# Kernel tuning notes

Hardware: AMD Instinct MI355X
Metric: run time of the kernel (lower is better)

Reference implementation:

```python
import jax, jax.numpy as jnp
import numpy as np
from jax import lax

B, C, H, W = 32, 128, 56, 56
O, KS, K = 128, 3, 2
HIDDEN = 32  # int(in_planes * ratio)
TEMPERATURE = 31.0
STRIDE, PAD = 1, 1


def setup_inputs() -> dict:
    key = jax.random.key(0)
    ks = jax.random.split(key, 6)
    return {
        "x": jax.random.normal(ks[0], (B, C, H, W), jnp.float32),
        "common_weight": jax.random.normal(ks[1], (1, O, C, KS, KS), jnp.float32) * 0.05,
        "common_bias": jax.random.normal(ks[2], (1, O), jnp.float32) * 0.05,
        "dyn_weight": jax.random.normal(ks[3], (1, O, C, KS, KS), jnp.float32) * 0.05,
        "dyn_bias": jnp.zeros((1, O), jnp.float32),
        "fc1_w": jax.random.normal(ks[4], (HIDDEN, C), jnp.float32) * 0.1,
        "fc2_w": jax.random.normal(ks[5], (K, HIDDEN), jnp.float32) * 0.1,
    }


def reference(x, common_weight, common_bias, dyn_weight, dyn_bias, fc1_w, fc2_w):
    b, c, h, w = x.shape
    # attention2d: global avg pool -> 1x1 conv -> relu -> 1x1 conv -> softmax(./T)
    pooled = jnp.mean(x, axis=(2, 3))                       # [B, C]
    hid = jax.nn.relu(pooled @ fc1_w.T)                     # [B, hidden]
    logits = hid @ fc2_w.T                                  # [B, K]
    attn = jax.nn.softmax(logits / TEMPERATURE, axis=1)     # [B, K]

    # aggregate per-sample weights/biases from the K-bank
    weight_all = jnp.concatenate([common_weight, dyn_weight], axis=0)  # [K,O,C,k,k]
    agg_w = jnp.einsum('bk,kocij->bocij', attn, weight_all)            # [B,O,C,k,k]
    bias_all = jnp.concatenate([common_bias, dyn_bias], axis=0)       # [K,O]
    agg_b = attn @ bias_all                                            # [B,O]

    # per-sample conv via grouped conv with feature_group_count = batch
    x1 = x.reshape(1, b * c, h, w)
    w1 = agg_w.reshape(b * O, c, KS, KS)
    out = lax.conv_general_dilated(
        x1, w1,
        window_strides=(STRIDE, STRIDE),
        padding=((PAD, PAD), (PAD, PAD)),
        dimension_numbers=('NCHW', 'OIHW', 'NCHW'),
        feature_group_count=b,
    )  # [1, B*O, H', W']
    out = out.reshape(b, O, out.shape[-2], out.shape[-1])
    return out + agg_b[:, :, None, None]
```

## Files before the change

### kernel.cpp

```cpp
#include <hip/hip_runtime.h>


#define B_ 32
#define C_ 128
#define O_ 128
#define SP_ 3136

typedef __bf16  bf16x8 __attribute__((ext_vector_type(8)));
typedef short   short8 __attribute__((ext_vector_type(8)));
typedef float   f32x4  __attribute__((ext_vector_type(4)));

__device__ __forceinline__ short f2bf(float f) {
  unsigned u = __float_as_uint(f);
  u += 0x7fffu + ((u >> 16) & 1u);
  return (short)(u >> 16);
}
__device__ __forceinline__ float bf2f(short s) {
  return __uint_as_float(((unsigned)(unsigned short)s) << 16);
}

#define GLOAD_LDS16(gp, lp)                                                     \
  __builtin_amdgcn_global_load_lds(                                             \
      (const __attribute__((address_space(1))) unsigned int*)(gp),              \
      (__attribute__((address_space(3))) unsigned int*)(lp), 16, 0, 0)

#define WS_PARTIAL_F 0
#define WS_ATTN_F    229376
#define WS_AGGB_F    229440
#define WS_ZERO_B    934144
#define WS_WB_B      935168
#define WS_XH_B      10372352

__global__ __launch_bounds__(256) void convert_k(const float* __restrict__ x,
                                                 short* __restrict__ xh,
                                                 float* __restrict__ partial) {
  const int h = blockIdx.x, b = blockIdx.y;
  const int tid = threadIdx.x;
  __shared__ short lc[C_ * 57];
  const float* xp = x + (size_t)b * C_ * SP_ + h * 56;
#pragma unroll
  for (int q = 0; q < 7; ++q) {
    int i = q * 256 + tid;
    int c = i / 14, w4 = (i - c * 14) * 4;
    float4 v = *reinterpret_cast<const float4*>(xp + (size_t)c * SP_ + w4);
    lc[c * 57 + w4 + 0] = f2bf(v.x);
    lc[c * 57 + w4 + 1] = f2bf(v.y);
    lc[c * 57 + w4 + 2] = f2bf(v.z);
    lc[c * 57 + w4 + 3] = f2bf(v.w);
  }
  __syncthreads();
  if (tid < C_) {
    float s = 0.f;
    for (int w = 0; w < 56; ++w) s += bf2f(lc[tid * 57 + w]);
    partial[((size_t)b * 56 + h) * C_ + tid] = s;
  }
  short* xo = xh + ((size_t)b * 56 + h) * 56 * C_;
  for (int u = tid; u < 896; u += 256) {
    int w = u >> 4, cp = (u & 15) * 8;
    short8 v;
#pragma unroll
    for (int k = 0; k < 8; ++k) v[k] = lc[(cp + k) * 57 + w];
    *reinterpret_cast<short8*>(xo + w * C_ + cp) = v;
  }
}

__global__ __launch_bounds__(256) void pool_attn_k(const float* __restrict__ partial,
                                                   const float* __restrict__ fc1,
                                                   const float* __restrict__ fc2,
                                                   const float* __restrict__ cbias,
                                                   const float* __restrict__ dbias,
                                                   float* __restrict__ attn,
                                                   float* __restrict__ aggb) {
  const int b = blockIdx.x, tid = threadIdx.x;
  __shared__ float red[256];
  __shared__ float pooled_s[C_];
  __shared__ float hid[32];
  __shared__ float lg[2];
  __shared__ float at[2];
  {
    const int c = tid & 127, half = tid >> 7;
    float s = 0.f;
    for (int hh = half * 28; hh < half * 28 + 28; ++hh)
      s += partial[((size_t)b * 56 + hh) * C_ + c];
    red[tid] = s;
  }
  __syncthreads();
  if (tid < C_) pooled_s[tid] = (red[tid] + red[tid + 128]) * (1.f / 3136.f);
  __syncthreads();
  {
    const int hd = tid >> 3, part = tid & 7;
    const float4* fa = reinterpret_cast<const float4*>(fc1 + hd * C_ + part * 16);
    const float4* pa = reinterpret_cast<const float4*>(pooled_s + part * 16);
    float s = 0.f;
#pragma unroll
    for (int i = 0; i < 4; ++i) {
      float4 f = fa[i], p = pa[i];
      s += f.x * p.x + f.y * p.y + f.z * p.z + f.w * p.w;
    }
    red[tid] = s;
  }
  __syncthreads();
  if (tid < 32) {
    float v = 0.f;
#pragma unroll
    for (int j = 0; j < 8; ++j) v += red[tid * 8 + j];
    hid[tid] = fmaxf(v, 0.f);
  }
  __syncthreads();
  if (tid < 64) red[tid] = hid[tid & 31] * fc2[tid];
  __syncthreads();
  if (tid < 2) {
    float l = 0.f;
#pragma unroll
    for (int hh = 0; hh < 32; ++hh) l += red[tid * 32 + hh];
    lg[tid] = l * (1.f / 31.f);
  }
  __syncthreads();
  if (tid == 0) {
    float m = fmaxf(lg[0], lg[1]);
    float e0 = __expf(lg[0] - m), e1 = __expf(lg[1] - m);
    float inv = 1.f / (e0 + e1);
    at[0] = e0 * inv; at[1] = e1 * inv;
    attn[b * 2] = at[0]; attn[b * 2 + 1] = at[1];
  }
  __syncthreads();
  if (tid < C_)
    aggb[b * O_ + tid] = at[0] * cbias[tid] + at[1] * dbias[tid];
}

__global__ __launch_bounds__(256) void wagg_k(const float* __restrict__ w0,
                                              const float* __restrict__ w1,
                                              const float* __restrict__ attn,
                                              short* __restrict__ Wb) {
  const int b = blockIdx.x >> 3, og = blockIdx.x & 7;
  const int o0 = og * 16;
  const int tid = threadIdx.x;
  const float a0 = attn[b * 2], a1 = attn[b * 2 + 1];
  __shared__ short wl[9 * 16 * C_];
#pragma unroll
  for (int it = 0; it < 8; ++it) {
    int r = it * 256 + tid;
    int o = o0 + (r >> 7), c = r & 127;
    size_t base = ((size_t)o * C_ + c) * 9;
#pragma unroll
    for (int j = 0; j < 9; ++j) {
      float v = a0 * w0[base + j] + a1 * w1[base + j];
      wl[j * 2048 + r] = f2bf(v);
    }
  }
  __syncthreads();
#pragma unroll
  for (int it = 0; it < 9; ++it) {
    int u = it * 256 + tid;
    int ij = u >> 8, v = (u & 255) * 8;
    *reinterpret_cast<short8*>(Wb + (((size_t)b * 9 + ij) * O_ + o0) * C_ + v) =
        *reinterpret_cast<const short8*>(&wl[ij * 2048 + v]);
  }
}

#define TPOS 348
#define BUNITS 1392
#define BBUF 22272
#define AOFF 44544
#define ABUF 8192
__global__ __launch_bounds__(256, 2) void conv3_k(const char* __restrict__ wsbase,
                                                  const float* __restrict__ aggb,
                                                  float* __restrict__ out) {
  const int flat = blockIdx.x;
  const int swz = (flat & 7) * 56 + (flat >> 3);
  const int b = swz / 14, ht = swz - b * 14;
  const int h0 = ht * 4;
  const int tid = threadIdx.x;
  const int lane = tid & 63, wv = tid >> 6;
  const int obase = (wv >> 1) * 64;
  const int nbase = (wv & 1) * 112;
  const int l15 = lane & 15, g = lane >> 4;

  __shared__ __align__(16) char xs[AOFF + 2 * ABUF];

  const char* gsrcB[6];
  bool gact[6];
#pragma unroll
  for (int it = 0; it < 6; ++it) {
    int u = tid + it * 256;
    gact[it] = (u < BUNITS);
    int uu = gact[it] ? u : 0;
    int pos = uu >> 2;
    int q = ((uu & 3) - (uu >> 4)) & 3;
    int r = pos / 58, wc = pos - r * 58;
    int h = h0 - 1 + r, w = wc - 1;
    bool val = (unsigned)h < 56u && (unsigned)w < 56u;
    gsrcB[it] = wsbase + (val ? (WS_XH_B + 2 * ((((b * 56 + h) * 56 + w) << 7) + q * 8))
                              : WS_ZERO_B);
  }
  const char* gsrcA[2];
#pragma unroll
  for (int it = 0; it < 2; ++it) {
    int u = tid + it * 256;
    int o = u >> 2;
    int q = ((u & 3) - (u >> 4)) & 3;
    gsrcA[it] = wsbase + WS_WB_B + 2 * ((size_t)b * 147456 + o * C_ + q * 8);
  }
  int aoffR[4];
#pragma unroll
  for (int m = 0; m < 4; ++m) {
    int o = obase + m * 16 + l15;
    aoffR[m] = (o << 6) + (((g + (o >> 2)) & 3) << 4);
  }
  int ptile[7];
#pragma unroll
  for (int n = 0; n < 7; ++n) {
    int p = nbase + n * 16 + l15;
    int hl = p / 56, wl = p - hl * 56;
    ptile[n] = (hl + 1) * 58 + (wl + 1);
  }

  f32x4 acc[4][7];
#pragma unroll
  for (int m = 0; m < 4; ++m)
#pragma unroll
    for (int n = 0; n < 7; ++n) acc[m][n] = f32x4{0.f, 0.f, 0.f, 0.f};

#pragma unroll
  for (int it = 0; it < 6; ++it)
    if (gact[it]) GLOAD_LDS16(gsrcB[it], xs + it * 4096 + wv * 1024);
#pragma unroll
  for (int it = 0; it < 2; ++it)
    GLOAD_LDS16(gsrcA[it], xs + AOFF + it * 4096 + wv * 1024);
  asm volatile("s_waitcnt vmcnt(0)" ::: "memory");
  __builtin_amdgcn_s_barrier();

#pragma unroll
  for (int cc = 0; cc < 4; ++cc) {
#pragma unroll
    for (int ij = 0; ij < 9; ++ij) {
      const int s = cc * 9 + ij;
      const int apar = s & 1, bpar = cc & 1;
      if (s < 35) {
        const int s2 = s + 1, cc2 = s2 / 9, ij2 = s2 - cc2 * 9;
        const int adelta = 2 * (ij2 * 16384 + cc2 * 32);
#pragma unroll
        for (int it = 0; it < 2; ++it)
          GLOAD_LDS16(gsrcA[it] + adelta,
                      xs + AOFF + ((s2 & 1) ? ABUF : 0) + it * 4096 + wv * 1024);
      }
      if (ij == 0 && cc < 3) {
#pragma unroll
        for (int it = 0; it < 6; ++it)
          if (gact[it])
            GLOAD_LDS16(gsrcB[it] + (cc + 1) * 64,
                        xs + (bpar ? 0 : BBUF) + it * 4096 + wv * 1024);
      }
      const char* abuf = xs + AOFF + (apar ? ABUF : 0);
      const char* bbuf = xs + (bpar ? BBUF : 0);
      bf16x8 af[4];
#pragma unroll
      for (int m = 0; m < 4; ++m)
        af[m] = *reinterpret_cast<const bf16x8*>(abuf + aoffR[m]);
      const int sh = (ij / 3 - 1) * 58 + (ij % 3 - 1);
#pragma unroll
      for (int n = 0; n < 7; ++n) {
        int pp = ptile[n] + sh;
        int off = (pp << 6) + ((((pp >> 2) + g) & 3) << 4);
        bf16x8 bfr = *reinterpret_cast<const bf16x8*>(bbuf + off);
#pragma unroll
        for (int m = 0; m < 4; ++m)
          acc[m][n] = __builtin_amdgcn_mfma_f32_16x16x32_bf16(af[m], bfr, acc[m][n], 0, 0, 0);
      }
      if (s < 35) {
        asm volatile("s_waitcnt vmcnt(0)" ::: "memory");
        __builtin_amdgcn_s_barrier();
      }
    }
  }

  const int r4 = g * 4;
#pragma unroll
  for (int m = 0; m < 4; ++m) {
    float bias[4];
#pragma unroll
    for (int j = 0; j < 4; ++j) bias[j] = aggb[b * O_ + obase + m * 16 + r4 + j];
#pragma unroll
    for (int n = 0; n < 7; ++n) {
      int p = nbase + n * 16 + l15;
      int h = h0 + p / 56, w = p % 56;
#pragma unroll
      for (int j = 0; j < 4; ++j) {
        int o = obase + m * 16 + r4 + j;
        out[((size_t)(b * O_ + o) * 56 + h) * 56 + w] = acc[m][n][j] + bias[j];
      }
    }
  }
}

extern "C" void kernel_launch(void* const* d_in, const int* in_sizes, int n_in,
                              void* d_out, int out_size, void* d_ws, size_t ws_size,
                              hipStream_t stream) {
  const float* x    = (const float*)d_in[0];
  const float* cw   = (const float*)d_in[1];
  const float* cb   = (const float*)d_in[2];
  const float* dw   = (const float*)d_in[3];
  const float* db   = (const float*)d_in[4];
  const float* fc1  = (const float*)d_in[5];
  const float* fc2  = (const float*)d_in[6];
  float* out = (float*)d_out;

  char* wsb      = (char*)d_ws;
  float* partial = (float*)wsb + WS_PARTIAL_F;
  float* attn    = (float*)wsb + WS_ATTN_F;
  float* aggb    = (float*)wsb + WS_AGGB_F;
  short* Wb      = (short*)(wsb + WS_WB_B);
  short* xh      = (short*)(wsb + WS_XH_B);

  hipMemsetAsync(wsb + WS_ZERO_B, 0, 1024, stream);
  convert_k<<<dim3(56, B_), 256, 0, stream>>>(x, xh, partial);
  pool_attn_k<<<B_, 256, 0, stream>>>(partial, fc1, fc2, cb, db, attn, aggb);
  wagg_k<<<256, 256, 0, stream>>>(cw, dw, attn, Wb);
  conv3_k<<<448, 256, 0, stream>>>(wsb, aggb, out);
}
```

Baseline: 175.4 us.

## Fuse attention into weight aggregation and split conv across eight waves

The pooled-attention computation moves into the weight-aggregation kernel, where each block recomputes its sample's attention, so one launch and the attn round trip through memory go away. The workspace memset is replaced by a write from one block of the convert kernel, and that kernel's row sum now uses both thread halves. The conv kernel now runs 512 threads per block, each wave owning a 32x112 output tile instead of 64x112, with raised MFMA priority around the compute loop. This trades fewer launches and more resident waves for redundant attention work, doubled B-fragment LDS reads per output, and register pressure from the tighter launch bounds that could cause spills.

```diff
diff --git a/kernel.cpp b/kernel.cpp
--- a/kernel.cpp
+++ b/kernel.cpp
@@ -25,18 +25,19 @@
       (__attribute__((address_space(3))) unsigned int*)(lp), 16, 0, 0)
 
 #define WS_PARTIAL_F 0
-#define WS_ATTN_F    229376
 #define WS_AGGB_F    229440
 #define WS_ZERO_B    934144
 #define WS_WB_B      935168
 #define WS_XH_B      10372352
 
 __global__ __launch_bounds__(256) void convert_k(const float* __restrict__ x,
-                                                 short* __restrict__ xh,
-                                                 float* __restrict__ partial) {
+                                                 char* __restrict__ wsbase) {
   const int h = blockIdx.x, b = blockIdx.y;
   const int tid = threadIdx.x;
   __shared__ short lc[C_ * 57];
+  __shared__ float red[256];
+  if (h == 0 && b == 0)
+    ((int*)(wsbase + WS_ZERO_B))[tid] = 0;
   const float* xp = x + (size_t)b * C_ * SP_ + h * 56;
 #pragma unroll
   for (int q = 0; q < 7; ++q) {
@@ -49,12 +50,19 @@
     lc[c * 57 + w4 + 3] = f2bf(v.w);
   }
   __syncthreads();
+  {
+    const int c = tid & 127, half = tid >> 7;
+    float s = 0.f;
+#pragma unroll
+    for (int w = half * 28; w < half * 28 + 28; ++w) s += bf2f(lc[c * 57 + w]);
+    red[tid] = s;
+  }
+  __syncthreads();
   if (tid < C_) {
-    float s = 0.f;
-    for (int w = 0; w < 56; ++w) s += bf2f(lc[tid * 57 + w]);
-    partial[((size_t)b * 56 + h) * C_ + tid] = s;
-  }
-  short* xo = xh + ((size_t)b * 56 + h) * 56 * C_;
+    float* partial = (float*)wsbase + WS_PARTIAL_F;
+    partial[((size_t)b * 56 + h) * C_ + tid] = red[tid] + red[tid + 128];
+  }
+  short* xo = (short*)(wsbase + WS_XH_B) + ((size_t)b * 56 + h) * 56 * C_;
   for (int u = tid; u < 896; u += 256) {
     int w = u >> 4, cp = (u & 15) * 8;
     short8 v;
@@ -64,19 +72,24 @@
   }
 }
 
-__global__ __launch_bounds__(256) void pool_attn_k(const float* __restrict__ partial,
-                                                   const float* __restrict__ fc1,
-                                                   const float* __restrict__ fc2,
-                                                   const float* __restrict__ cbias,
-                                                   const float* __restrict__ dbias,
-                                                   float* __restrict__ attn,
-                                                   float* __restrict__ aggb) {
-  const int b = blockIdx.x, tid = threadIdx.x;
+__global__ __launch_bounds__(256) void wagg2_k(const float* __restrict__ w0,
+                                               const float* __restrict__ w1,
+                                               const float* __restrict__ fc1,
+                                               const float* __restrict__ fc2,
+                                               const float* __restrict__ cbias,
+                                               const float* __restrict__ dbias,
+                                               char* __restrict__ wsbase) {
+  const int b = blockIdx.x >> 3, og = blockIdx.x & 7;
+  const int o0 = og * 16;
+  const int tid = threadIdx.x;
+  const float* partial = (const float*)wsbase + WS_PARTIAL_F;
   __shared__ float red[256];
   __shared__ float pooled_s[C_];
   __shared__ float hid[32];
   __shared__ float lg[2];
   __shared__ float at[2];
+  __shared__ short wl[9 * 16 * C_];
+
   {
     const int c = tid & 127, half = tid >> 7;
     float s = 0.f;
@@ -121,22 +134,13 @@
     float e0 = __expf(lg[0] - m), e1 = __expf(lg[1] - m);
     float inv = 1.f / (e0 + e1);
     at[0] = e0 * inv; at[1] = e1 * inv;
-    attn[b * 2] = at[0]; attn[b * 2 + 1] = at[1];
-  }
-  __syncthreads();
-  if (tid < C_)
-    aggb[b * O_ + tid] = at[0] * cbias[tid] + at[1] * dbias[tid];
-}
-
-__global__ __launch_bounds__(256) void wagg_k(const float* __restrict__ w0,
-                                              const float* __restrict__ w1,
-                                              const float* __restrict__ attn,
-                                              short* __restrict__ Wb) {
-  const int b = blockIdx.x >> 3, og = blockIdx.x & 7;
-  const int o0 = og * 16;
-  const int tid = threadIdx.x;
-  const float a0 = attn[b * 2], a1 = attn[b * 2 + 1];
-  __shared__ short wl[9 * 16 * C_];
+  }
+  __syncthreads();
+  const float a0 = at[0], a1 = at[1];
+  if (og == 0 && tid < C_) {
+    float* aggb = (float*)wsbase + WS_AGGB_F;
+    aggb[b * O_ + tid] = a0 * cbias[tid] + a1 * dbias[tid];
+  }
 #pragma unroll
   for (int it = 0; it < 8; ++it) {
     int r = it * 256 + tid;
@@ -149,6 +153,7 @@
     }
   }
   __syncthreads();
+  short* Wb = (short*)(wsbase + WS_WB_B);
 #pragma unroll
   for (int it = 0; it < 9; ++it) {
     int u = it * 256 + tid;
@@ -158,13 +163,11 @@
   }
 }
 
-#define TPOS 348
 #define BUNITS 1392
 #define BBUF 22272
 #define AOFF 44544
 #define ABUF 8192
-__global__ __launch_bounds__(256, 2) void conv3_k(const char* __restrict__ wsbase,
-                                                  const float* __restrict__ aggb,
+__global__ __launch_bounds__(512, 4) void conv4_k(const char* __restrict__ wsbase,
                                                   float* __restrict__ out) {
   const int flat = blockIdx.x;
   const int swz = (flat & 7) * 56 + (flat >> 3);
@@ -172,17 +175,18 @@
   const int h0 = ht * 4;
   const int tid = threadIdx.x;
   const int lane = tid & 63, wv = tid >> 6;
-  const int obase = (wv >> 1) * 64;
+  const int obase = (wv >> 1) * 32;
   const int nbase = (wv & 1) * 112;
   const int l15 = lane & 15, g = lane >> 4;
+  const float* aggb = (const float*)wsbase + WS_AGGB_F;
 
   __shared__ __align__(16) char xs[AOFF + 2 * ABUF];
 
-  const char* gsrcB[6];
-  bool gact[6];
-#pragma unroll
-  for (int it = 0; it < 6; ++it) {
-    int u = tid + it * 256;
+  const char* gsrcB[3];
+  bool gact[3];
+#pragma unroll
+  for (int it = 0; it < 3; ++it) {
+    int u = it * 512 + tid;
     gact[it] = (u < BUNITS);
     int uu = gact[it] ? u : 0;
     int pos = uu >> 2;
@@ -193,17 +197,15 @@
     gsrcB[it] = wsbase + (val ? (WS_XH_B + 2 * ((((b * 56 + h) * 56 + w) << 7) + q * 8))
                               : WS_ZERO_B);
   }
-  const char* gsrcA[2];
-#pragma unroll
-  for (int it = 0; it < 2; ++it) {
-    int u = tid + it * 256;
-    int o = u >> 2;
-    int q = ((u & 3) - (u >> 4)) & 3;
-    gsrcA[it] = wsbase + WS_WB_B + 2 * ((size_t)b * 147456 + o * C_ + q * 8);
-  }
-  int aoffR[4];
-#pragma unroll
-  for (int m = 0; m < 4; ++m) {
+  const char* gsrcA;
+  {
+    int o = tid >> 2;
+    int q = ((tid & 3) - (tid >> 4)) & 3;
+    gsrcA = wsbase + WS_WB_B + 2 * ((size_t)b * 147456 + o * C_ + q * 8);
+  }
+  int aoffR[2];
+#pragma unroll
+  for (int m = 0; m < 2; ++m) {
     int o = obase + m * 16 + l15;
     aoffR[m] = (o << 6) + (((g + (o >> 2)) & 3) << 4);
   }
@@ -215,18 +217,16 @@
     ptile[n] = (hl + 1) * 58 + (wl + 1);
   }
 
-  f32x4 acc[4][7];
-#pragma unroll
-  for (int m = 0; m < 4; ++m)
+  f32x4 acc[2][7];
+#pragma unroll
+  for (int m = 0; m < 2; ++m)
 #pragma unroll
     for (int n = 0; n < 7; ++n) acc[m][n] = f32x4{0.f, 0.f, 0.f, 0.f};
 
 #pragma unroll
-  for (int it = 0; it < 6; ++it)
-    if (gact[it]) GLOAD_LDS16(gsrcB[it], xs + it * 4096 + wv * 1024);
-#pragma unroll
-  for (int it = 0; it < 2; ++it)
-    GLOAD_LDS16(gsrcA[it], xs + AOFF + it * 4096 + wv * 1024);
+  for (int it = 0; it < 3; ++it)
+    if (gact[it]) GLOAD_LDS16(gsrcB[it], xs + it * 8192 + wv * 1024);
+  GLOAD_LDS16(gsrcA, xs + AOFF + wv * 1024);
   asm volatile("s_waitcnt vmcnt(0)" ::: "memory");
   __builtin_amdgcn_s_barrier();
 
@@ -238,35 +238,34 @@
       const int apar = s & 1, bpar = cc & 1;
       if (s < 35) {
         const int s2 = s + 1, cc2 = s2 / 9, ij2 = s2 - cc2 * 9;
-        const int adelta = 2 * (ij2 * 16384 + cc2 * 32);
-#pragma unroll
-        for (int it = 0; it < 2; ++it)
-          GLOAD_LDS16(gsrcA[it] + adelta,
-                      xs + AOFF + ((s2 & 1) ? ABUF : 0) + it * 4096 + wv * 1024);
+        GLOAD_LDS16(gsrcA + 2 * (ij2 * 16384 + cc2 * 32),
+                    xs + AOFF + ((s2 & 1) ? ABUF : 0) + wv * 1024);
       }
       if (ij == 0 && cc < 3) {
 #pragma unroll
-        for (int it = 0; it < 6; ++it)
+        for (int it = 0; it < 3; ++it)
           if (gact[it])
             GLOAD_LDS16(gsrcB[it] + (cc + 1) * 64,
-                        xs + (bpar ? 0 : BBUF) + it * 4096 + wv * 1024);
+                        xs + (bpar ? 0 : BBUF) + it * 8192 + wv * 1024);
       }
       const char* abuf = xs + AOFF + (apar ? ABUF : 0);
       const char* bbuf = xs + (bpar ? BBUF : 0);
-      bf16x8 af[4];
-#pragma unroll
-      for (int m = 0; m < 4; ++m)
+      bf16x8 af[2];
+#pragma unroll
+      for (int m = 0; m < 2; ++m)
         af[m] = *reinterpret_cast<const bf16x8*>(abuf + aoffR[m]);
       const int sh = (ij / 3 - 1) * 58 + (ij % 3 - 1);
+      __builtin_amdgcn_s_setprio(1);
 #pragma unroll
       for (int n = 0; n < 7; ++n) {
         int pp = ptile[n] + sh;
         int off = (pp << 6) + ((((pp >> 2) + g) & 3) << 4);
         bf16x8 bfr = *reinterpret_cast<const bf16x8*>(bbuf + off);
 #pragma unroll
-        for (int m = 0; m < 4; ++m)
+        for (int m = 0; m < 2; ++m)
           acc[m][n] = __builtin_amdgcn_mfma_f32_16x16x32_bf16(af[m], bfr, acc[m][n], 0, 0, 0);
       }
+      __builtin_amdgcn_s_setprio(0);
       if (s < 35) {
         asm volatile("s_waitcnt vmcnt(0)" ::: "memory");
         __builtin_amdgcn_s_barrier();
@@ -276,7 +275,7 @@
 
   const int r4 = g * 4;
 #pragma unroll
-  for (int m = 0; m < 4; ++m) {
+  for (int m = 0; m < 2; ++m) {
     float bias[4];
 #pragma unroll
     for (int j = 0; j < 4; ++j) bias[j] = aggb[b * O_ + obase + m * 16 + r4 + j];
@@ -296,25 +295,17 @@
 extern "C" void kernel_launch(void* const* d_in, const int* in_sizes, int n_in,
                               void* d_out, int out_size, void* d_ws, size_t ws_size,
                               hipStream_t stream) {
-  const float* x    = (const float*)d_in[0];
-  const float* cw   = (const float*)d_in[1];
-  const float* cb   = (const float*)d_in[2];
-  const float* dw   = (const float*)d_in[3];
-  const float* db   = (const float*)d_in[4];
-  const float* fc1  = (const float*)d_in[5];
-  const float* fc2  = (const float*)d_in[6];
+  const float* x   = (const float*)d_in[0];
+  const float* cw  = (const float*)d_in[1];
+  const float* cb  = (const float*)d_in[2];
+  const float* dw  = (const float*)d_in[3];
+  const float* db  = (const float*)d_in[4];
+  const float* fc1 = (const float*)d_in[5];
+  const float* fc2 = (const float*)d_in[6];
   float* out = (float*)d_out;
-
-  char* wsb      = (char*)d_ws;
-  float* partial = (float*)wsb + WS_PARTIAL_F;
-  float* attn    = (float*)wsb + WS_ATTN_F;
-  float* aggb    = (float*)wsb + WS_AGGB_F;
-  short* Wb      = (short*)(wsb + WS_WB_B);
-  short* xh      = (short*)(wsb + WS_XH_B);
-
-  hipMemsetAsync(wsb + WS_ZERO_B, 0, 1024, stream);
-  convert_k<<<dim3(56, B_), 256, 0, stream>>>(x, xh, partial);
-  pool_attn_k<<<B_, 256, 0, stream>>>(partial, fc1, fc2, cb, db, attn, aggb);
-  wagg_k<<<256, 256, 0, stream>>>(cw, dw, attn, Wb);
-  conv3_k<<<448, 256, 0, stream>>>(wsb, aggb, out);
-}
+  char* wsb  = (char*)d_ws;
+
+  convert_k<<<dim3(56, B_), 256, 0, stream>>>(x, wsb);
+  wagg2_k<<<256, 256, 0, stream>>>(cw, dw, fc1, fc2, cb, db, wsb);
+  conv4_k<<<448, 512, 0, stream>>>(wsb, out);
+}
```

Measured after the change: 230.1 us. 31.2% more time.
